# Performance work log

Measured on AMD Instinct MI355X. Metric: run time of the kernel, lower is better.

## Reference

```python
import jax, jax.numpy as jnp
import numpy as np

N, E, D, H = 100000, 20000, 64, 4
NNZ = 500000
NEG_SLOPE_ATT = 0.2   # PyG HypergraphConv attention leaky_relu slope
NEG_SLOPE_FFN = 0.01  # nn.LeakyReLU default
LN_EPS = 1e-5


def setup_inputs() -> dict:
    key = jax.random.key(0)
    ks = jax.random.split(key, 10)
    s = 0.05
    return {
        "x": jax.random.normal(ks[0], (N, D), jnp.float32),
        "adj_row": jax.random.randint(ks[1], (NNZ,), 0, N),
        "adj_col": jax.random.randint(ks[2], (NNZ,), 0, E),
        "adj_val": jax.random.uniform(ks[3], (NNZ,), jnp.float32) + 0.1,
        "num_edges": E,
        "lin_w": jax.random.normal(ks[4], (H * D, D), jnp.float32) * s,
        "att": jax.random.normal(ks[5], (1, H, 2 * D), jnp.float32) * s,
        "bias": jnp.zeros((D,), jnp.float32),
        "ln1_g": jnp.ones((D,), jnp.float32),
        "ln1_b": jnp.zeros((D,), jnp.float32),
        "ln2_g": jnp.ones((D,), jnp.float32),
        "ln2_b": jnp.zeros((D,), jnp.float32),
        "w1": jax.random.normal(ks[6], (D, D), jnp.float32) * s,
        "b1": jnp.zeros((D,), jnp.float32),
        "w2": jax.random.normal(ks[7], (D, D), jnp.float32) * s,
        "b2": jnp.zeros((D,), jnp.float32),
    }


def _layer_norm(x, g, b):
    mu = jnp.mean(x, axis=-1, keepdims=True)
    var = jnp.mean((x - mu) ** 2, axis=-1, keepdims=True)
    return (x - mu) * jax.lax.rsqrt(var + LN_EPS) * g + b


def _hypergraph_layer(x, adj_row, adj_col, adj_val, num_edges,
                      lin_w, att, bias, ln1_g, ln1_b, ln2_g, ln2_b,
                      w1, b1, w2, b2):
    n = x.shape[0]
    # --- get_hyperedge_representation: omega = diag(1/colsum) @ H^T @ x ---
    colsum = jax.ops.segment_sum(adj_val, adj_col, num_segments=num_edges)  # [E]
    omega = jax.ops.segment_sum(adj_val[:, None] * x[adj_row], adj_col,
                                num_segments=num_edges) / colsum[:, None]  # [E, D]
    # --- HypergraphConv (use_attention=True, concat=False) ---
    xh = (x @ lin_w.T).reshape(n, H, D)              # [N, H, D]
    eh = (omega @ lin_w.T).reshape(num_edges, H, D)  # [E, H, D]
    att_x, att_e = att[0, :, :D], att[0, :, D:]      # [H, D] each
    s_n = jnp.einsum('nhd,hd->nh', xh, att_x)        # [N, H]
    s_e = jnp.einsum('ehd,hd->eh', eh, att_e)        # [E, H]
    alpha = jax.nn.leaky_relu(s_n[adj_row] + s_e[adj_col], NEG_SLOPE_ATT)  # [NNZ, H]
    # softmax over incidences grouped by hyperedge (attention_mode='node')
    amax = jax.ops.segment_max(alpha, adj_col, num_segments=num_edges)
    ea = jnp.exp(alpha - amax[adj_col])
    alpha = ea / jax.ops.segment_sum(ea, adj_col, num_segments=num_edges)[adj_col]
    # degree normalizations D (node) and B (hyperedge)
    d_deg = jax.ops.segment_sum(adj_val[adj_col], adj_row, num_segments=n)
    d_inv = jnp.where(d_deg > 0, 1.0 / d_deg, 0.0)
    b_deg = jax.ops.segment_sum(jnp.ones_like(adj_val), adj_col, num_segments=num_edges)
    b_inv = jnp.where(b_deg > 0, 1.0 / b_deg, 0.0)
    # pass 1: nodes -> hyperedges  (norm_i = B at target edge)
    msg1 = b_inv[adj_col][:, None, None] * xh[adj_row] * alpha[:, :, None]
    edge_out = jax.ops.segment_sum(msg1, adj_col, num_segments=num_edges)  # [E,H,D]
    # pass 2: hyperedges -> nodes  (norm_i = D at target node)
    msg2 = d_inv[adj_row][:, None, None] * edge_out[adj_col] * alpha[:, :, None]
    node_out = jax.ops.segment_sum(msg2, adj_row, num_segments=n)  # [N,H,D]
    conv = jnp.mean(node_out, axis=1) + bias  # concat=False -> head mean
    # --- residual + norm + FFN (Linear, Linear, LeakyReLU) ---
    h = _layer_norm(x + conv, ln1_g, ln1_b)
    ffn = jax.nn.leaky_relu((h @ w1.T + b1) @ w2.T + b2, NEG_SLOPE_FFN)
    return _layer_norm(h + ffn, ln2_g, ln2_b)


def reference(x, adj_row, adj_col, adj_val, num_edges, lin_w, att, bias,
              ln1_g, ln1_b, ln2_g, ln2_b, w1, b1, w2, b2):
    return _hypergraph_layer(x, adj_row, adj_col, adj_val, num_edges,
                             lin_w, att, bias, ln1_g, ln1_b, ln2_g, ln2_b,
                             w1, b1, w2, b2)
```

## Files before the change

### kernel.cpp

```cpp
#include <hip/hip_runtime.h>

#define N_NODES 100000
#define N_EDGES 20000
#define DIM 64
#define HEADS 4
#define NNZ_ 500000
#define LNEPS 1e-5f

__device__ __forceinline__ float wsum64(float v){
#pragma unroll
  for (int off = 32; off; off >>= 1) v += __shfl_xor(v, off);
  return v;
}
__device__ __forceinline__ float wmax64(float v){
#pragma unroll
  for (int off = 32; off; off >>= 1) v = fmaxf(v, __shfl_xor(v, off));
  return v;
}
__device__ __forceinline__ float lrelu2(float a){ return a > 0.f ? a : 0.2f*a; }

__device__ __forceinline__ unsigned bfpack(float a, float b){
  unsigned ua = __float_as_uint(a), ub = __float_as_uint(b);
  ua += 0x7fffu + ((ua >> 16) & 1u);
  ub += 0x7fffu + ((ub >> 16) & 1u);
  return (ua >> 16) | (ub & 0xffff0000u);
}

__global__ __launch_bounds__(256) void k_hist(const int* __restrict__ row,
                                              const int* __restrict__ col,
                                              const float* __restrict__ val,
                                              int* __restrict__ ecnt, int* __restrict__ ncnt,
                                              float* __restrict__ colsum, float* __restrict__ ddeg){
  int i = blockIdx.x*256 + threadIdx.x;
  if (i >= NNZ_) return;
  int c = col[i], r = row[i];
  atomicAdd(&ecnt[c], 1);
  atomicAdd(&ncnt[r], 1);
  atomicAdd(&colsum[c], val[i]);
  atomicAdd(&ddeg[r], val[c]);
}

__global__ __launch_bounds__(1024) void k_scanA(const int* __restrict__ cnt,
                                                int* __restrict__ ptr,
                                                int* __restrict__ bsum, int n){
  __shared__ int wsums[16];
  int idx = blockIdx.x*1024 + threadIdx.x;
  int lane = threadIdx.x & 63, wid = threadIdx.x >> 6;
  int v = (idx < n) ? cnt[idx] : 0;
  int s = v;
#pragma unroll
  for (int off = 1; off < 64; off <<= 1){
    int t = __shfl_up(s, off);
    if (lane >= off) s += t;
  }
  if (lane == 63) wsums[wid] = s;
  __syncthreads();
  if (wid == 0 && lane < 16){
    int ws = wsums[lane];
    int t = ws;
#pragma unroll
    for (int off = 1; off < 16; off <<= 1){
      int u = __shfl_up(t, off);
      if (lane >= off) t += u;
    }
    wsums[lane] = t - ws;
  }
  __syncthreads();
  if (idx < n) ptr[idx] = wsums[wid] + s - v;
  if (threadIdx.x == 1023) bsum[blockIdx.x] = wsums[15] + s;
}

__global__ __launch_bounds__(256) void k_scanB(int* __restrict__ bsum, int nb,
                                               int* __restrict__ ptr, int n){
  __shared__ int sh[256];
  int t = threadIdx.x;
  int v = (t < nb) ? bsum[t] : 0;
  sh[t] = v;
  __syncthreads();
  for (int off = 1; off < 256; off <<= 1){
    int u = (t >= off) ? sh[t-off] : 0;
    __syncthreads();
    sh[t] += u;
    __syncthreads();
  }
  if (t < nb) bsum[t] = sh[t] - v;
  if (t == nb-1) ptr[n] = sh[t];
}

__global__ __launch_bounds__(1024) void k_scanC(int* __restrict__ ptr,
                                                const int* __restrict__ bsum, int n){
  int idx = blockIdx.x*1024 + threadIdx.x;
  if (idx < n) ptr[idx] += bsum[blockIdx.x];
}

__global__ __launch_bounds__(256) void k_scatter(const int* __restrict__ row,
                                                 const int* __restrict__ col,
                                                 const float* __restrict__ val,
                                                 const int* __restrict__ colptr,
                                                 const int* __restrict__ rowptr,
                                                 int* __restrict__ ecur, int* __restrict__ ncur,
                                                 int* __restrict__ rowC, float* __restrict__ valC,
                                                 int* __restrict__ rposC, int* __restrict__ colR){
  int i = blockIdx.x*256 + threadIdx.x;
  if (i >= NNZ_) return;
  int c = col[i], r = row[i];
  int p = atomicAdd(&ecur[c], 1);
  int q = atomicAdd(&ncur[r], 1);
  int cpos = colptr[c] + p;
  int rpos = rowptr[r] + q;
  rowC[cpos] = r;
  valC[cpos] = val[i];
  rposC[cpos] = rpos;
  colR[rpos] = c;
}

__global__ __launch_bounds__(256) void k_watt(const float* __restrict__ lin_w,
                                              const float* __restrict__ att,
                                              float* __restrict__ wattx,
                                              float* __restrict__ watte){
  int j = threadIdx.x;
  int h = j >> 6;
  float sx = 0.f, se = 0.f;
#pragma unroll
  for (int d = 0; d < DIM; ++d){
    float w = lin_w[(h*DIM + d)*DIM + (j & 63)];
    sx = fmaf(att[h*2*DIM + d],       w, sx);
    se = fmaf(att[h*2*DIM + DIM + d], w, se);
  }
  wattx[j] = sx;
  watte[j] = se;
}

__global__ __launch_bounds__(256) void k_wfold(const float* __restrict__ w1,
                                               const float* __restrict__ w2,
                                               const float* __restrict__ b1,
                                               const float* __restrict__ b2,
                                               float* __restrict__ Wf,
                                               float* __restrict__ bp){
  int tid = threadIdx.x;
#pragma unroll
  for (int m = 0; m < 16; ++m){
    int idx = m*256 + tid;
    int o = idx >> 6, k = idx & 63;
    float s = 0.f;
#pragma unroll
    for (int i = 0; i < 64; ++i)
      s = fmaf(w2[o*64 + i], w1[i*64 + k], s);
    Wf[idx] = s;
  }
  if (tid < 64){
    float s = b2[tid];
#pragma unroll
    for (int i = 0; i < 64; ++i)
      s = fmaf(w2[tid*64 + i], b1[i], s);
    bp[tid] = s;
  }
}

__global__ __launch_bounds__(256) void k_pre(const float* __restrict__ x,
                                             const float* __restrict__ wattx,
                                             const float* __restrict__ watte,
                                             float4* __restrict__ snpe){
  int lane = threadIdx.x & 63, wid = threadIdx.x >> 6;
  int n = blockIdx.x*4 + wid;
  if (n >= N_NODES) return;
  float xv = x[(size_t)n*DIM + lane];
  float s0 = wsum64(xv*wattx[lane]);
  float s1 = wsum64(xv*wattx[64+lane]);
  float s2 = wsum64(xv*wattx[128+lane]);
  float s3 = wsum64(xv*wattx[192+lane]);
  float p0 = wsum64(xv*watte[lane]);
  float p1 = wsum64(xv*watte[64+lane]);
  float p2 = wsum64(xv*watte[128+lane]);
  float p3 = wsum64(xv*watte[192+lane]);
  if (lane == 0){
    snpe[2*(size_t)n    ] = make_float4(s0,s1,s2,s3);
    snpe[2*(size_t)n + 1] = make_float4(p0,p1,p2,p3);
  }
}

__global__ __launch_bounds__(256) void k_softagg(const int* __restrict__ colptr,
                                                 const int* __restrict__ rowC,
                                                 const float* __restrict__ valC,
                                                 const int* __restrict__ rposC,
                                                 const float4* __restrict__ snpe,
                                                 const float* __restrict__ colsum,
                                                 const float* __restrict__ x,
                                                 float4* __restrict__ alphaC,
                                                 float4* __restrict__ alphaR,
                                                 float* __restrict__ agg){
  __shared__ float4 aSh[256];
  int lane = threadIdx.x & 63, wid = threadIdx.x >> 6;
  int e = blockIdx.x*4 + wid;
  if (e >= N_EDGES) return;
  int sb = __builtin_amdgcn_readfirstlane(colptr[e]);
  int cnt = __builtin_amdgcn_readfirstlane(colptr[e+1]) - sb;
  if (cnt == 0) return;
  float rcs = 1.0f / colsum[e];
  float acc0=0,acc1=0,acc2=0,acc3=0;

  if (cnt <= 64){
    bool act = lane < cnt;
    int r = 0, rp = 0; float v = 0.f;
    float4 snv = make_float4(0,0,0,0), p = make_float4(0,0,0,0);
    if (act){
      r = rowC[sb+lane];
      v = valC[sb+lane];
      rp = rposC[sb+lane];
      snv = snpe[2*(size_t)r];
      p   = snpe[2*(size_t)r + 1];
    }
    float se0 = wsum64(v*p.x)*rcs, se1 = wsum64(v*p.y)*rcs,
          se2 = wsum64(v*p.z)*rcs, se3 = wsum64(v*p.w)*rcs;
    float t0 = act ? lrelu2(snv.x+se0) : -1e30f;
    float t1 = act ? lrelu2(snv.y+se1) : -1e30f;
    float t2 = act ? lrelu2(snv.z+se2) : -1e30f;
    float t3 = act ? lrelu2(snv.w+se3) : -1e30f;
    float m0 = wmax64(t0), m1 = wmax64(t1), m2 = wmax64(t2), m3 = wmax64(t3);
    float e0 = act ? __expf(t0-m0) : 0.f;
    float e1 = act ? __expf(t1-m1) : 0.f;
    float e2 = act ? __expf(t2-m2) : 0.f;
    float e3 = act ? __expf(t3-m3) : 0.f;
    float q0 = wsum64(e0), q1 = wsum64(e1), q2 = wsum64(e2), q3 = wsum64(e3);
    float4 a = make_float4(e0/q0, e1/q1, e2/q2, e3/q3);
    if (act) alphaR[rp] = a;
    aSh[wid*64 + lane] = a;

    int k = 0;
    for (; k + 4 <= cnt; k += 4){
      int r0 = rowC[sb+k], r1 = rowC[sb+k+1], r2 = rowC[sb+k+2], r3 = rowC[sb+k+3];
      float4 a0 = aSh[wid*64+k], a1 = aSh[wid*64+k+1],
             a2 = aSh[wid*64+k+2], a3 = aSh[wid*64+k+3];
      float x0 = x[(size_t)r0*DIM + lane];
      float x1 = x[(size_t)r1*DIM + lane];
      float x2 = x[(size_t)r2*DIM + lane];
      float x3 = x[(size_t)r3*DIM + lane];
      acc0 = fmaf(a0.x, x0, acc0); acc1 = fmaf(a0.y, x0, acc1);
      acc2 = fmaf(a0.z, x0, acc2); acc3 = fmaf(a0.w, x0, acc3);
      acc0 = fmaf(a1.x, x1, acc0); acc1 = fmaf(a1.y, x1, acc1);
      acc2 = fmaf(a1.z, x1, acc2); acc3 = fmaf(a1.w, x1, acc3);
      acc0 = fmaf(a2.x, x2, acc0); acc1 = fmaf(a2.y, x2, acc1);
      acc2 = fmaf(a2.z, x2, acc2); acc3 = fmaf(a2.w, x2, acc3);
      acc0 = fmaf(a3.x, x3, acc0); acc1 = fmaf(a3.y, x3, acc1);
      acc2 = fmaf(a3.z, x3, acc2); acc3 = fmaf(a3.w, x3, acc3);
    }
    for (; k < cnt; ++k){
      int r0 = rowC[sb+k];
      float4 a0 = aSh[wid*64+k];
      float x0 = x[(size_t)r0*DIM + lane];
      acc0 = fmaf(a0.x, x0, acc0); acc1 = fmaf(a0.y, x0, acc1);
      acc2 = fmaf(a0.z, x0, acc2); acc3 = fmaf(a0.w, x0, acc3);
    }
  } else {
    int s = sb;
    float a0=0,a1=0,a2=0,a3=0;
    for (int base = 0; base < cnt; base += 64){
      int j = s + base + lane;
      if (base + lane < cnt){
        int r = rowC[j]; float v = valC[j];
        float4 p = snpe[2*(size_t)r + 1];
        a0 = fmaf(v,p.x,a0); a1 = fmaf(v,p.y,a1); a2 = fmaf(v,p.z,a2); a3 = fmaf(v,p.w,a3);
      }
    }
    float se0 = wsum64(a0)*rcs, se1 = wsum64(a1)*rcs, se2 = wsum64(a2)*rcs, se3 = wsum64(a3)*rcs;
    float m0=-1e30f,m1=-1e30f,m2=-1e30f,m3=-1e30f;
    for (int base = 0; base < cnt; base += 64){
      int j = s + base + lane;
      if (base + lane < cnt){
        float4 snv = snpe[2*(size_t)rowC[j]];
        m0 = fmaxf(m0, lrelu2(snv.x+se0)); m1 = fmaxf(m1, lrelu2(snv.y+se1));
        m2 = fmaxf(m2, lrelu2(snv.z+se2)); m3 = fmaxf(m3, lrelu2(snv.w+se3));
      }
    }
    m0 = wmax64(m0); m1 = wmax64(m1); m2 = wmax64(m2); m3 = wmax64(m3);
    float q0=0,q1=0,q2=0,q3=0;
    for (int base = 0; base < cnt; base += 64){
      int j = s + base + lane;
      if (base + lane < cnt){
        float4 snv = snpe[2*(size_t)rowC[j]];
        float e0 = __expf(lrelu2(snv.x+se0)-m0), e1 = __expf(lrelu2(snv.y+se1)-m1);
        float e2 = __expf(lrelu2(snv.z+se2)-m2), e3 = __expf(lrelu2(snv.w+se3)-m3);
        q0+=e0; q1+=e1; q2+=e2; q3+=e3;
        alphaC[j] = make_float4(e0,e1,e2,e3);
      }
    }
    q0 = wsum64(q0); q1 = wsum64(q1); q2 = wsum64(q2); q3 = wsum64(q3);
    float r0 = 1.f/q0, r1 = 1.f/q1, r2 = 1.f/q2, r3 = 1.f/q3;
    for (int base = 0; base < cnt; base += 64){
      int j = s + base + lane;
      if (base + lane < cnt){
        float4 av = alphaC[j];
        av = make_float4(av.x*r0, av.y*r1, av.z*r2, av.w*r3);
        alphaC[j] = av;
        alphaR[rposC[j]] = av;
      }
    }
    for (int k = 0; k < cnt; ++k){
      int rj = rowC[sb+k];
      float4 al = alphaC[sb+k];
      float xv = x[(size_t)rj*DIM + lane];
      acc0 = fmaf(al.x, xv, acc0); acc1 = fmaf(al.y, xv, acc1);
      acc2 = fmaf(al.z, xv, acc2); acc3 = fmaf(al.w, xv, acc3);
    }
  }

  float binv = 1.0f/(float)cnt;
  size_t b = (size_t)e*256;
  agg[b       + lane] = acc0*binv;
  agg[b +  64 + lane] = acc1*binv;
  agg[b + 128 + lane] = acc2*binv;
  agg[b + 192 + lane] = acc3*binv;
}

__global__ __launch_bounds__(256) void k_eoT(const float* __restrict__ agg,
                                             const float* __restrict__ lin_w,
                                             unsigned short* __restrict__ eoTb){
  __shared__ float L[16*260];
  int lane = threadIdx.x & 63, h = threadIdx.x >> 6;
  float w[64];
  const float4* wr = (const float4*)(lin_w + ((size_t)h*64 + lane)*64);
#pragma unroll
  for (int k = 0; k < 16; ++k){
    float4 t = wr[k];
    w[4*k] = t.x; w[4*k+1] = t.y; w[4*k+2] = t.z; w[4*k+3] = t.w;
  }
  int e0 = blockIdx.x*16;
  for (int el = 0; el < 16; ++el){
    float av = agg[(size_t)(e0+el)*256 + h*64 + lane];
    float o = 0.f;
#pragma unroll
    for (int k = 0; k < 64; ++k) o = fmaf(__shfl(av, k), w[k], o);
    L[el*260 + lane*4 + h] = o;
  }
  __syncthreads();
  int tid = threadIdx.x;
#pragma unroll
  for (int p = 0; p < 4; ++p){
    int el = p*4 + (tid >> 6);
    int l = tid & 63;
    const float* Lr = &L[el*260 + l*4];
    uint2 v;
    v.x = bfpack(Lr[0], Lr[1]);
    v.y = bfpack(Lr[2], Lr[3]);
    *(uint2*)(eoTb + (size_t)(e0+el)*256 + l*4) = v;
  }
}

#define ACC4(J, V, A) { \
  float u0 = __uint_as_float((V).x << 16); \
  float u1 = __uint_as_float((V).x & 0xffff0000u); \
  float u2 = __uint_as_float((V).y << 16); \
  float u3 = __uint_as_float((V).y & 0xffff0000u); \
  acc[J][0] = fmaf(u0, (A).x, acc[J][0]); \
  acc[J][1] = fmaf(u1, (A).y, acc[J][1]); \
  acc[J][2] = fmaf(u2, (A).z, acc[J][2]); \
  acc[J][3] = fmaf(u3, (A).w, acc[J][3]); }

#define SEG(J, KB, KE) do { \
    int k = (KB); \
    for (; k + 4 <= (KE); k += 4){ \
      int c0 = colR[k], c1 = colR[k+1], c2 = colR[k+2], c3 = colR[k+3]; \
      float4 a0 = alphaR[k], a1 = alphaR[k+1], a2 = alphaR[k+2], a3 = alphaR[k+3]; \
      uint2 v0 = *(const uint2*)(eoTb + (size_t)c0*256 + lane*4); \
      uint2 v1 = *(const uint2*)(eoTb + (size_t)c1*256 + lane*4); \
      uint2 v2 = *(const uint2*)(eoTb + (size_t)c2*256 + lane*4); \
      uint2 v3 = *(const uint2*)(eoTb + (size_t)c3*256 + lane*4); \
      ACC4(J, v0, a0); ACC4(J, v1, a1); ACC4(J, v2, a2); ACC4(J, v3, a3); \
    } \
    for (; k < (KE); ++k){ \
      int c0 = colR[k]; float4 a0 = alphaR[k]; \
      uint2 v0 = *(const uint2*)(eoTb + (size_t)c0*256 + lane*4); \
      ACC4(J, v0, a0); \
    } \
  } while(0)

__global__ __launch_bounds__(256) void k_final2(const float* __restrict__ x,
                                                const int* __restrict__ rowptr,
                                                const int* __restrict__ colR,
                                                const float4* __restrict__ alphaR,
                                                const unsigned short* __restrict__ eoTb,
                                                const float* __restrict__ ddeg,
                                                const float* __restrict__ bias,
                                                const float* __restrict__ g1,
                                                const float* __restrict__ b1g,
                                                const float* __restrict__ g2,
                                                const float* __restrict__ b2g,
                                                const float* __restrict__ Wf,
                                                const float* __restrict__ bp,
                                                float* __restrict__ out){
  int lane = threadIdx.x & 63, wid = threadIdx.x >> 6;
  int nbase = blockIdx.x*16 + wid*4;
  int q0 = __builtin_amdgcn_readfirstlane(rowptr[nbase]);
  int q1 = __builtin_amdgcn_readfirstlane(rowptr[nbase+1]);
  int q2 = __builtin_amdgcn_readfirstlane(rowptr[nbase+2]);
  int q3 = __builtin_amdgcn_readfirstlane(rowptr[nbase+3]);
  int q4 = __builtin_amdgcn_readfirstlane(rowptr[nbase+4]);

  float xv[4];
#pragma unroll
  for (int j = 0; j < 4; ++j) xv[j] = x[(size_t)(nbase+j)*DIM + lane];
  float dd0 = ddeg[nbase], dd1 = ddeg[nbase+1], dd2 = ddeg[nbase+2], dd3 = ddeg[nbase+3];
  float w[64];
  const float4* wr = (const float4*)(Wf + (size_t)lane*64);
#pragma unroll
  for (int k = 0; k < 16; ++k){
    float4 t = wr[k];
    w[4*k] = t.x; w[4*k+1] = t.y; w[4*k+2] = t.z; w[4*k+3] = t.w;
  }
  float biasv = bias[lane], bpv = bp[lane];
  float g1v = g1[lane], b1gv = b1g[lane], g2v = g2[lane], b2gv = b2g[lane];

  float acc[4][4];
#pragma unroll
  for (int j = 0; j < 4; ++j)
#pragma unroll
    for (int h = 0; h < 4; ++h) acc[j][h] = 0.f;

  SEG(0, q0, q1);
  SEG(1, q1, q2);
  SEG(2, q2, q3);
  SEG(3, q3, q4);

  float ddv[4] = {dd0, dd1, dd2, dd3};
  float hs[4];
#pragma unroll
  for (int j = 0; j < 4; ++j){
    float dd = ddv[j];
    float dinv = dd > 0.f ? 0.25f/dd : 0.f;
    float conv = (acc[j][0]+acc[j][1]+acc[j][2]+acc[j][3])*dinv;
    float t = xv[j] + conv + biasv;
    float mu = wsum64(t) * (1.f/64.f);
    float dv = t - mu;
    float var = wsum64(dv*dv) * (1.f/64.f);
    hs[j] = dv * rsqrtf(var + LNEPS) * g1v + b1gv;
  }

  float a0 = bpv, a1 = bpv, a2 = bpv, a3 = bpv;
#pragma unroll
  for (int k = 0; k < 64; ++k){
    a0 = fmaf(__shfl(hs[0], k), w[k], a0);
    a1 = fmaf(__shfl(hs[1], k), w[k], a1);
    a2 = fmaf(__shfl(hs[2], k), w[k], a2);
    a3 = fmaf(__shfl(hs[3], k), w[k], a3);
  }

  float fa[4] = {a0, a1, a2, a3};
#pragma unroll
  for (int j = 0; j < 4; ++j){
    int n = nbase + j;
    float ffn = fa[j] > 0.f ? fa[j] : 0.01f*fa[j];
    float t2 = hs[j] + ffn;
    float mu2 = wsum64(t2) * (1.f/64.f);
    float dv2 = t2 - mu2;
    float var2 = wsum64(dv2*dv2) * (1.f/64.f);
    out[(size_t)n*DIM + lane] = dv2 * rsqrtf(var2 + LNEPS) * g2v + b2gv;
  }
}

extern "C" void kernel_launch(void* const* d_in, const int* in_sizes, int n_in,
                              void* d_out, int out_size, void* d_ws, size_t ws_size,
                              hipStream_t stream){
  const float* x     = (const float*)d_in[0];
  const int*   row   = (const int*)d_in[1];
  const int*   col   = (const int*)d_in[2];
  const float* val   = (const float*)d_in[3];
  const float* lin_w = (const float*)d_in[5];
  const float* att   = (const float*)d_in[6];
  const float* bias  = (const float*)d_in[7];
  const float* g1    = (const float*)d_in[8];
  const float* b1g   = (const float*)d_in[9];
  const float* g2    = (const float*)d_in[10];
  const float* b2g   = (const float*)d_in[11];
  const float* w1    = (const float*)d_in[12];
  const float* b1    = (const float*)d_in[13];
  const float* w2    = (const float*)d_in[14];
  const float* b2    = (const float*)d_in[15];
  float* out = (float*)d_out;
  float* ws  = (float*)d_ws;

  constexpr size_t E = N_EDGES, Nn = N_NODES;
  constexpr size_t o_ecnt   = 0;
  constexpr size_t o_ncnt   = o_ecnt + E;
  constexpr size_t o_ecur   = o_ncnt + Nn;
  constexpr size_t o_ncur   = o_ecur + E;
  constexpr size_t o_colsum = o_ncur + Nn;
  constexpr size_t o_ddeg   = o_colsum + E;
  constexpr size_t ZEND     = o_ddeg + Nn;
  constexpr size_t o_colptr = ZEND;
  constexpr size_t o_rowptr = o_colptr + E + 4;
  constexpr size_t o_bsumE  = o_rowptr + Nn + 4;
  constexpr size_t o_bsumN  = o_bsumE + 256;
  constexpr size_t o_rowC   = o_bsumN + 256;
  constexpr size_t o_valC   = o_rowC + NNZ_;
  constexpr size_t o_rposC  = o_valC + NNZ_;
  constexpr size_t o_colR   = o_rposC + NNZ_;
  constexpr size_t o_wattx  = o_colR + NNZ_;
  constexpr size_t o_watte  = o_wattx + 256;
  constexpr size_t o_Wf     = o_watte + 256;
  constexpr size_t o_bp     = o_Wf + 4096;
  constexpr size_t o_snpe   = o_bp + 64;
  constexpr size_t o_alphaC = o_snpe + 8*Nn;
  constexpr size_t o_alphaR = o_alphaC + 4*(size_t)NNZ_;
  constexpr size_t o_agg    = o_alphaR + 4*(size_t)NNZ_;
  constexpr size_t o_eo     = o_agg + 256*E;

  int*    ecnt   = (int*)(ws + o_ecnt);
  int*    ncnt   = (int*)(ws + o_ncnt);
  int*    ecur   = (int*)(ws + o_ecur);
  int*    ncur   = (int*)(ws + o_ncur);
  float*  colsum = ws + o_colsum;
  float*  ddeg   = ws + o_ddeg;
  int*    colptr = (int*)(ws + o_colptr);
  int*    rowptr = (int*)(ws + o_rowptr);
  int*    bsumE  = (int*)(ws + o_bsumE);
  int*    bsumN  = (int*)(ws + o_bsumN);
  int*    rowC   = (int*)(ws + o_rowC);
  float*  valC   = ws + o_valC;
  int*    rposC  = (int*)(ws + o_rposC);
  int*    colR   = (int*)(ws + o_colR);
  float*  wattx  = ws + o_wattx;
  float*  watte  = ws + o_watte;
  float*  Wf     = ws + o_Wf;
  float*  bp     = ws + o_bp;
  float4* snpe   = (float4*)(ws + o_snpe);
  float4* alphaC = (float4*)(ws + o_alphaC);
  float4* alphaR = (float4*)(ws + o_alphaR);
  float*  agg    = ws + o_agg;
  unsigned short* eoTb = (unsigned short*)(ws + o_eo);

  hipMemsetAsync(ws, 0, ZEND*sizeof(float), stream);

  k_hist<<<(NNZ_+255)/256, 256, 0, stream>>>(row, col, val, ecnt, ncnt, colsum, ddeg);

  int nbE = (int)((E + 1023)/1024);
  int nbN = (int)((Nn + 1023)/1024);
  k_scanA<<<nbE, 1024, 0, stream>>>(ecnt, colptr, bsumE, (int)E);
  k_scanB<<<1, 256, 0, stream>>>(bsumE, nbE, colptr, (int)E);
  k_scanC<<<nbE, 1024, 0, stream>>>(colptr, bsumE, (int)E);
  k_scanA<<<nbN, 1024, 0, stream>>>(ncnt, rowptr, bsumN, (int)Nn);
  k_scanB<<<1, 256, 0, stream>>>(bsumN, nbN, rowptr, (int)Nn);
  k_scanC<<<nbN, 1024, 0, stream>>>(rowptr, bsumN, (int)Nn);

  k_scatter<<<(NNZ_+255)/256, 256, 0, stream>>>(row, col, val, colptr, rowptr,
                                                ecur, ncur, rowC, valC, rposC, colR);

  k_watt<<<1, 256, 0, stream>>>(lin_w, att, wattx, watte);
  k_wfold<<<1, 256, 0, stream>>>(w1, w2, b1, b2, Wf, bp);
  k_pre<<<(int)((Nn+3)/4), 256, 0, stream>>>(x, wattx, watte, snpe);
  k_softagg<<<(int)((E+3)/4), 256, 0, stream>>>(colptr, rowC, valC, rposC, snpe, colsum,
                                                x, alphaC, alphaR, agg);
  k_eoT<<<(int)(E/16), 256, 0, stream>>>(agg, lin_w, eoTb);
  k_final2<<<(int)(Nn/16), 256, 0, stream>>>(x, rowptr, colR, alphaR, eoTb, ddeg,
                                             bias, g1, b1g, g2, b2g, Wf, bp, out);
}
```

Before: 452.6 us.

## Merge edge/node scan launches, unroll eoT over 4 edges, one node per wave in final

The separate edge and node prefix-scan kernels are merged into three combined launches, which cuts launch count and serialization. k_eoT now processes four edges per inner iteration so one weight register value feeds four FMAs. k_final2 switches from four nodes per wave to one node per wave with four times as many blocks. This exposes more parallelism and balances load across irregular row lengths, at the cost of reloading the 64-float weight row per node instead of amortizing it over four.

```diff
diff --git a/kernel.cpp b/kernel.cpp
--- a/kernel.cpp
+++ b/kernel.cpp
@@ -40,11 +40,10 @@
   atomicAdd(&ddeg[r], val[c]);
 }
 
-__global__ __launch_bounds__(1024) void k_scanA(const int* __restrict__ cnt,
-                                                int* __restrict__ ptr,
-                                                int* __restrict__ bsum, int n){
+__device__ __forceinline__ void scanA_body(const int* cnt, int* ptr, int* bsum,
+                                           int n, int blk){
   __shared__ int wsums[16];
-  int idx = blockIdx.x*1024 + threadIdx.x;
+  int idx = blk*1024 + threadIdx.x;
   int lane = threadIdx.x & 63, wid = threadIdx.x >> 6;
   int v = (idx < n) ? cnt[idx] : 0;
   int s = v;
@@ -67,11 +66,21 @@
   }
   __syncthreads();
   if (idx < n) ptr[idx] = wsums[wid] + s - v;
-  if (threadIdx.x == 1023) bsum[blockIdx.x] = wsums[15] + s;
-}
-
-__global__ __launch_bounds__(256) void k_scanB(int* __restrict__ bsum, int nb,
-                                               int* __restrict__ ptr, int n){
+  if (threadIdx.x == 1023) bsum[blk] = wsums[15] + s;
+}
+
+__global__ __launch_bounds__(1024) void k_scanA2(const int* __restrict__ ecnt,
+                                                 int* __restrict__ colptr,
+                                                 int* __restrict__ bsumE, int nbE,
+                                                 const int* __restrict__ ncnt,
+                                                 int* __restrict__ rowptr,
+                                                 int* __restrict__ bsumN){
+  int b = blockIdx.x;
+  if (b < nbE) scanA_body(ecnt, colptr, bsumE, N_EDGES, b);
+  else         scanA_body(ncnt, rowptr, bsumN, N_NODES, b - nbE);
+}
+
+__device__ __forceinline__ void scanB_body(int* bsum, int nb, int* ptr, int n){
   __shared__ int sh[256];
   int t = threadIdx.x;
   int v = (t < nb) ? bsum[t] : 0;
@@ -87,10 +96,26 @@
   if (t == nb-1) ptr[n] = sh[t];
 }
 
-__global__ __launch_bounds__(1024) void k_scanC(int* __restrict__ ptr,
-                                                const int* __restrict__ bsum, int n){
-  int idx = blockIdx.x*1024 + threadIdx.x;
-  if (idx < n) ptr[idx] += bsum[blockIdx.x];
+__global__ __launch_bounds__(256) void k_scanB2(int* __restrict__ bsumE, int nbE,
+                                                int* __restrict__ colptr,
+                                                int* __restrict__ bsumN, int nbN,
+                                                int* __restrict__ rowptr){
+  if (blockIdx.x == 0) scanB_body(bsumE, nbE, colptr, N_EDGES);
+  else                 scanB_body(bsumN, nbN, rowptr, N_NODES);
+}
+
+__global__ __launch_bounds__(1024) void k_scanC2(int* __restrict__ colptr,
+                                                 const int* __restrict__ bsumE, int nbE,
+                                                 int* __restrict__ rowptr,
+                                                 const int* __restrict__ bsumN){
+  int b = blockIdx.x;
+  if (b < nbE){
+    int idx = b*1024 + threadIdx.x;
+    if (idx < N_EDGES) colptr[idx] += bsumE[b];
+  } else {
+    int idx = (b - nbE)*1024 + threadIdx.x;
+    if (idx < N_NODES) rowptr[idx] += bsumN[b - nbE];
+  }
 }
 
 __global__ __launch_bounds__(256) void k_scatter(const int* __restrict__ row,
@@ -325,12 +350,25 @@
     w[4*k] = t.x; w[4*k+1] = t.y; w[4*k+2] = t.z; w[4*k+3] = t.w;
   }
   int e0 = blockIdx.x*16;
-  for (int el = 0; el < 16; ++el){
-    float av = agg[(size_t)(e0+el)*256 + h*64 + lane];
-    float o = 0.f;
-#pragma unroll
-    for (int k = 0; k < 64; ++k) o = fmaf(__shfl(av, k), w[k], o);
-    L[el*260 + lane*4 + h] = o;
+#pragma unroll
+  for (int el = 0; el < 16; el += 4){
+    float av0 = agg[(size_t)(e0+el  )*256 + h*64 + lane];
+    float av1 = agg[(size_t)(e0+el+1)*256 + h*64 + lane];
+    float av2 = agg[(size_t)(e0+el+2)*256 + h*64 + lane];
+    float av3 = agg[(size_t)(e0+el+3)*256 + h*64 + lane];
+    float o0=0.f, o1=0.f, o2=0.f, o3=0.f;
+#pragma unroll
+    for (int k = 0; k < 64; ++k){
+      float wk = w[k];
+      o0 = fmaf(__shfl(av0, k), wk, o0);
+      o1 = fmaf(__shfl(av1, k), wk, o1);
+      o2 = fmaf(__shfl(av2, k), wk, o2);
+      o3 = fmaf(__shfl(av3, k), wk, o3);
+    }
+    L[(el  )*260 + lane*4 + h] = o0;
+    L[(el+1)*260 + lane*4 + h] = o1;
+    L[(el+2)*260 + lane*4 + h] = o2;
+    L[(el+3)*260 + lane*4 + h] = o3;
   }
   __syncthreads();
   int tid = threadIdx.x;
@@ -346,33 +384,15 @@
   }
 }
 
-#define ACC4(J, V, A) { \
+#define ACC1(V, A) { \
   float u0 = __uint_as_float((V).x << 16); \
   float u1 = __uint_as_float((V).x & 0xffff0000u); \
   float u2 = __uint_as_float((V).y << 16); \
   float u3 = __uint_as_float((V).y & 0xffff0000u); \
-  acc[J][0] = fmaf(u0, (A).x, acc[J][0]); \
-  acc[J][1] = fmaf(u1, (A).y, acc[J][1]); \
-  acc[J][2] = fmaf(u2, (A).z, acc[J][2]); \
-  acc[J][3] = fmaf(u3, (A).w, acc[J][3]); }
-
-#define SEG(J, KB, KE) do { \
-    int k = (KB); \
-    for (; k + 4 <= (KE); k += 4){ \
-      int c0 = colR[k], c1 = colR[k+1], c2 = colR[k+2], c3 = colR[k+3]; \
-      float4 a0 = alphaR[k], a1 = alphaR[k+1], a2 = alphaR[k+2], a3 = alphaR[k+3]; \
-      uint2 v0 = *(const uint2*)(eoTb + (size_t)c0*256 + lane*4); \
-      uint2 v1 = *(const uint2*)(eoTb + (size_t)c1*256 + lane*4); \
-      uint2 v2 = *(const uint2*)(eoTb + (size_t)c2*256 + lane*4); \
-      uint2 v3 = *(const uint2*)(eoTb + (size_t)c3*256 + lane*4); \
-      ACC4(J, v0, a0); ACC4(J, v1, a1); ACC4(J, v2, a2); ACC4(J, v3, a3); \
-    } \
-    for (; k < (KE); ++k){ \
-      int c0 = colR[k]; float4 a0 = alphaR[k]; \
-      uint2 v0 = *(const uint2*)(eoTb + (size_t)c0*256 + lane*4); \
-      ACC4(J, v0, a0); \
-    } \
-  } while(0)
+  acc0 = fmaf(u0, (A).x, acc0); \
+  acc1 = fmaf(u1, (A).y, acc1); \
+  acc2 = fmaf(u2, (A).z, acc2); \
+  acc3 = fmaf(u3, (A).w, acc3); }
 
 __global__ __launch_bounds__(256) void k_final2(const float* __restrict__ x,
                                                 const int* __restrict__ rowptr,
@@ -389,72 +409,59 @@
                                                 const float* __restrict__ bp,
                                                 float* __restrict__ out){
   int lane = threadIdx.x & 63, wid = threadIdx.x >> 6;
-  int nbase = blockIdx.x*16 + wid*4;
-  int q0 = __builtin_amdgcn_readfirstlane(rowptr[nbase]);
-  int q1 = __builtin_amdgcn_readfirstlane(rowptr[nbase+1]);
-  int q2 = __builtin_amdgcn_readfirstlane(rowptr[nbase+2]);
-  int q3 = __builtin_amdgcn_readfirstlane(rowptr[nbase+3]);
-  int q4 = __builtin_amdgcn_readfirstlane(rowptr[nbase+4]);
-
-  float xv[4];
-#pragma unroll
-  for (int j = 0; j < 4; ++j) xv[j] = x[(size_t)(nbase+j)*DIM + lane];
-  float dd0 = ddeg[nbase], dd1 = ddeg[nbase+1], dd2 = ddeg[nbase+2], dd3 = ddeg[nbase+3];
+  int n = blockIdx.x*4 + wid;
+  int q0 = __builtin_amdgcn_readfirstlane(rowptr[n]);
+  int q1 = __builtin_amdgcn_readfirstlane(rowptr[n+1]);
+
+  float xv = x[(size_t)n*DIM + lane];
+  float dd = ddeg[n];
+
+  float acc0=0.f, acc1=0.f, acc2=0.f, acc3=0.f;
+  int k = q0;
+  for (; k + 4 <= q1; k += 4){
+    int c0 = colR[k], c1 = colR[k+1], c2 = colR[k+2], c3 = colR[k+3];
+    float4 a0 = alphaR[k], a1 = alphaR[k+1], a2 = alphaR[k+2], a3 = alphaR[k+3];
+    uint2 v0 = *(const uint2*)(eoTb + (size_t)c0*256 + lane*4);
+    uint2 v1 = *(const uint2*)(eoTb + (size_t)c1*256 + lane*4);
+    uint2 v2 = *(const uint2*)(eoTb + (size_t)c2*256 + lane*4);
+    uint2 v3 = *(const uint2*)(eoTb + (size_t)c3*256 + lane*4);
+    ACC1(v0, a0); ACC1(v1, a1); ACC1(v2, a2); ACC1(v3, a3);
+  }
+  for (; k < q1; ++k){
+    int c0 = colR[k]; float4 a0 = alphaR[k];
+    uint2 v0 = *(const uint2*)(eoTb + (size_t)c0*256 + lane*4);
+    ACC1(v0, a0);
+  }
+
   float w[64];
   const float4* wr = (const float4*)(Wf + (size_t)lane*64);
 #pragma unroll
-  for (int k = 0; k < 16; ++k){
-    float4 t = wr[k];
-    w[4*k] = t.x; w[4*k+1] = t.y; w[4*k+2] = t.z; w[4*k+3] = t.w;
+  for (int kk = 0; kk < 16; ++kk){
+    float4 t = wr[kk];
+    w[4*kk] = t.x; w[4*kk+1] = t.y; w[4*kk+2] = t.z; w[4*kk+3] = t.w;
   }
   float biasv = bias[lane], bpv = bp[lane];
   float g1v = g1[lane], b1gv = b1g[lane], g2v = g2[lane], b2gv = b2g[lane];
 
-  float acc[4][4];
-#pragma unroll
-  for (int j = 0; j < 4; ++j)
-#pragma unroll
-    for (int h = 0; h < 4; ++h) acc[j][h] = 0.f;
-
-  SEG(0, q0, q1);
-  SEG(1, q1, q2);
-  SEG(2, q2, q3);
-  SEG(3, q3, q4);
-
-  float ddv[4] = {dd0, dd1, dd2, dd3};
-  float hs[4];
-#pragma unroll
-  for (int j = 0; j < 4; ++j){
-    float dd = ddv[j];
-    float dinv = dd > 0.f ? 0.25f/dd : 0.f;
-    float conv = (acc[j][0]+acc[j][1]+acc[j][2]+acc[j][3])*dinv;
-    float t = xv[j] + conv + biasv;
-    float mu = wsum64(t) * (1.f/64.f);
-    float dv = t - mu;
-    float var = wsum64(dv*dv) * (1.f/64.f);
-    hs[j] = dv * rsqrtf(var + LNEPS) * g1v + b1gv;
-  }
-
-  float a0 = bpv, a1 = bpv, a2 = bpv, a3 = bpv;
-#pragma unroll
-  for (int k = 0; k < 64; ++k){
-    a0 = fmaf(__shfl(hs[0], k), w[k], a0);
-    a1 = fmaf(__shfl(hs[1], k), w[k], a1);
-    a2 = fmaf(__shfl(hs[2], k), w[k], a2);
-    a3 = fmaf(__shfl(hs[3], k), w[k], a3);
-  }
-
-  float fa[4] = {a0, a1, a2, a3};
-#pragma unroll
-  for (int j = 0; j < 4; ++j){
-    int n = nbase + j;
-    float ffn = fa[j] > 0.f ? fa[j] : 0.01f*fa[j];
-    float t2 = hs[j] + ffn;
-    float mu2 = wsum64(t2) * (1.f/64.f);
-    float dv2 = t2 - mu2;
-    float var2 = wsum64(dv2*dv2) * (1.f/64.f);
-    out[(size_t)n*DIM + lane] = dv2 * rsqrtf(var2 + LNEPS) * g2v + b2gv;
-  }
+  float dinv = dd > 0.f ? 0.25f/dd : 0.f;
+  float conv = (acc0+acc1+acc2+acc3)*dinv;
+  float t = xv + conv + biasv;
+  float mu = wsum64(t) * (1.f/64.f);
+  float dv = t - mu;
+  float var = wsum64(dv*dv) * (1.f/64.f);
+  float hv = dv * rsqrtf(var + LNEPS) * g1v + b1gv;
+
+  float a = bpv;
+#pragma unroll
+  for (int kk = 0; kk < 64; ++kk)
+    a = fmaf(__shfl(hv, kk), w[kk], a);
+
+  float ffn = a > 0.f ? a : 0.01f*a;
+  float t2 = hv + ffn;
+  float mu2 = wsum64(t2) * (1.f/64.f);
+  float dv2 = t2 - mu2;
+  float var2 = wsum64(dv2*dv2) * (1.f/64.f);
+  out[(size_t)n*DIM + lane] = dv2 * rsqrtf(var2 + LNEPS) * g2v + b2gv;
 }
 
 extern "C" void kernel_launch(void* const* d_in, const int* in_sizes, int n_in,
@@ -534,12 +541,9 @@
 
   int nbE = (int)((E + 1023)/1024);
   int nbN = (int)((Nn + 1023)/1024);
-  k_scanA<<<nbE, 1024, 0, stream>>>(ecnt, colptr, bsumE, (int)E);
-  k_scanB<<<1, 256, 0, stream>>>(bsumE, nbE, colptr, (int)E);
-  k_scanC<<<nbE, 1024, 0, stream>>>(colptr, bsumE, (int)E);
-  k_scanA<<<nbN, 1024, 0, stream>>>(ncnt, rowptr, bsumN, (int)Nn);
-  k_scanB<<<1, 256, 0, stream>>>(bsumN, nbN, rowptr, (int)Nn);
-  k_scanC<<<nbN, 1024, 0, stream>>>(rowptr, bsumN, (int)Nn);
+  k_scanA2<<<nbE + nbN, 1024, 0, stream>>>(ecnt, colptr, bsumE, nbE, ncnt, rowptr, bsumN);
+  k_scanB2<<<2, 256, 0, stream>>>(bsumE, nbE, colptr, bsumN, nbN, rowptr);
+  k_scanC2<<<nbE + nbN, 1024, 0, stream>>>(colptr, bsumE, nbE, rowptr, bsumN);
 
   k_scatter<<<(NNZ_+255)/256, 256, 0, stream>>>(row, col, val, colptr, rowptr,
                                                 ecur, ncur, rowC, valC, rposC, colR);
@@ -550,6 +554,6 @@
   k_softagg<<<(int)((E+3)/4), 256, 0, stream>>>(colptr, rowC, valC, rposC, snpe, colsum,
                                                 x, alphaC, alphaR, agg);
   k_eoT<<<(int)(E/16), 256, 0, stream>>>(agg, lin_w, eoTb);
-  k_final2<<<(int)(Nn/16), 256, 0, stream>>>(x, rowptr, colR, alphaR, eoTb, ddeg,
-                                             bias, g1, b1g, g2, b2g, Wf, bp, out);
-}
+  k_final2<<<(int)(Nn/4), 256, 0, stream>>>(x, rowptr, colR, alphaR, eoTb, ddeg,
+                                            bias, g1, b1g, g2, b2g, Wf, bp, out);
+}
```

Result: slower. 548.8 us (+21.3%).

## Merge scan kernels, shrink block sizes, unroll eoT over four edges

Applied to the files above, without the earlier changes.

Fuses the separate edge and node prefix-scan launches into three combined kernels, cutting the launch count from six to three. Halves the block size of k_pre, k_softagg and k_final2 so more, smaller blocks are scheduled. Reworks k_eoT to process four edges per inner loop, reusing each weight register across them. Moves the Wf register load in k_final2 after the gather loop to shorten register live ranges. The extra accumulators in k_eoT raise register pressure, and smaller blocks add scheduling overhead.

```diff
diff --git a/kernel.cpp b/kernel.cpp
--- a/kernel.cpp
+++ b/kernel.cpp
@@ -40,11 +40,10 @@
   atomicAdd(&ddeg[r], val[c]);
 }
 
-__global__ __launch_bounds__(1024) void k_scanA(const int* __restrict__ cnt,
-                                                int* __restrict__ ptr,
-                                                int* __restrict__ bsum, int n){
+__device__ __forceinline__ void scanA_body(const int* cnt, int* ptr, int* bsum,
+                                           int n, int blk){
   __shared__ int wsums[16];
-  int idx = blockIdx.x*1024 + threadIdx.x;
+  int idx = blk*1024 + threadIdx.x;
   int lane = threadIdx.x & 63, wid = threadIdx.x >> 6;
   int v = (idx < n) ? cnt[idx] : 0;
   int s = v;
@@ -67,11 +66,21 @@
   }
   __syncthreads();
   if (idx < n) ptr[idx] = wsums[wid] + s - v;
-  if (threadIdx.x == 1023) bsum[blockIdx.x] = wsums[15] + s;
-}
-
-__global__ __launch_bounds__(256) void k_scanB(int* __restrict__ bsum, int nb,
-                                               int* __restrict__ ptr, int n){
+  if (threadIdx.x == 1023) bsum[blk] = wsums[15] + s;
+}
+
+__global__ __launch_bounds__(1024) void k_scanA2(const int* __restrict__ ecnt,
+                                                 int* __restrict__ colptr,
+                                                 int* __restrict__ bsumE, int nbE,
+                                                 const int* __restrict__ ncnt,
+                                                 int* __restrict__ rowptr,
+                                                 int* __restrict__ bsumN){
+  int b = blockIdx.x;
+  if (b < nbE) scanA_body(ecnt, colptr, bsumE, N_EDGES, b);
+  else         scanA_body(ncnt, rowptr, bsumN, N_NODES, b - nbE);
+}
+
+__device__ __forceinline__ void scanB_body(int* bsum, int nb, int* ptr, int n){
   __shared__ int sh[256];
   int t = threadIdx.x;
   int v = (t < nb) ? bsum[t] : 0;
@@ -87,10 +96,26 @@
   if (t == nb-1) ptr[n] = sh[t];
 }
 
-__global__ __launch_bounds__(1024) void k_scanC(int* __restrict__ ptr,
-                                                const int* __restrict__ bsum, int n){
-  int idx = blockIdx.x*1024 + threadIdx.x;
-  if (idx < n) ptr[idx] += bsum[blockIdx.x];
+__global__ __launch_bounds__(256) void k_scanB2(int* __restrict__ bsumE, int nbE,
+                                                int* __restrict__ colptr,
+                                                int* __restrict__ bsumN, int nbN,
+                                                int* __restrict__ rowptr){
+  if (blockIdx.x == 0) scanB_body(bsumE, nbE, colptr, N_EDGES);
+  else                 scanB_body(bsumN, nbN, rowptr, N_NODES);
+}
+
+__global__ __launch_bounds__(1024) void k_scanC2(int* __restrict__ colptr,
+                                                 const int* __restrict__ bsumE, int nbE,
+                                                 int* __restrict__ rowptr,
+                                                 const int* __restrict__ bsumN){
+  int b = blockIdx.x;
+  if (b < nbE){
+    int idx = b*1024 + threadIdx.x;
+    if (idx < N_EDGES) colptr[idx] += bsumE[b];
+  } else {
+    int idx = (b - nbE)*1024 + threadIdx.x;
+    if (idx < N_NODES) rowptr[idx] += bsumN[b - nbE];
+  }
 }
 
 __global__ __launch_bounds__(256) void k_scatter(const int* __restrict__ row,
@@ -157,12 +182,12 @@
   }
 }
 
-__global__ __launch_bounds__(256) void k_pre(const float* __restrict__ x,
+__global__ __launch_bounds__(128) void k_pre(const float* __restrict__ x,
                                              const float* __restrict__ wattx,
                                              const float* __restrict__ watte,
                                              float4* __restrict__ snpe){
   int lane = threadIdx.x & 63, wid = threadIdx.x >> 6;
-  int n = blockIdx.x*4 + wid;
+  int n = blockIdx.x*2 + wid;
   if (n >= N_NODES) return;
   float xv = x[(size_t)n*DIM + lane];
   float s0 = wsum64(xv*wattx[lane]);
@@ -179,7 +204,7 @@
   }
 }
 
-__global__ __launch_bounds__(256) void k_softagg(const int* __restrict__ colptr,
+__global__ __launch_bounds__(128) void k_softagg(const int* __restrict__ colptr,
                                                  const int* __restrict__ rowC,
                                                  const float* __restrict__ valC,
                                                  const int* __restrict__ rposC,
@@ -189,9 +214,9 @@
                                                  float4* __restrict__ alphaC,
                                                  float4* __restrict__ alphaR,
                                                  float* __restrict__ agg){
-  __shared__ float4 aSh[256];
+  __shared__ float4 aSh[128];
   int lane = threadIdx.x & 63, wid = threadIdx.x >> 6;
-  int e = blockIdx.x*4 + wid;
+  int e = blockIdx.x*2 + wid;
   if (e >= N_EDGES) return;
   int sb = __builtin_amdgcn_readfirstlane(colptr[e]);
   int cnt = __builtin_amdgcn_readfirstlane(colptr[e+1]) - sb;
@@ -325,12 +350,25 @@
     w[4*k] = t.x; w[4*k+1] = t.y; w[4*k+2] = t.z; w[4*k+3] = t.w;
   }
   int e0 = blockIdx.x*16;
-  for (int el = 0; el < 16; ++el){
-    float av = agg[(size_t)(e0+el)*256 + h*64 + lane];
-    float o = 0.f;
-#pragma unroll
-    for (int k = 0; k < 64; ++k) o = fmaf(__shfl(av, k), w[k], o);
-    L[el*260 + lane*4 + h] = o;
+#pragma unroll
+  for (int el = 0; el < 16; el += 4){
+    float av0 = agg[(size_t)(e0+el  )*256 + h*64 + lane];
+    float av1 = agg[(size_t)(e0+el+1)*256 + h*64 + lane];
+    float av2 = agg[(size_t)(e0+el+2)*256 + h*64 + lane];
+    float av3 = agg[(size_t)(e0+el+3)*256 + h*64 + lane];
+    float o0=0.f, o1=0.f, o2=0.f, o3=0.f;
+#pragma unroll
+    for (int k = 0; k < 64; ++k){
+      float wk = w[k];
+      o0 = fmaf(__shfl(av0, k), wk, o0);
+      o1 = fmaf(__shfl(av1, k), wk, o1);
+      o2 = fmaf(__shfl(av2, k), wk, o2);
+      o3 = fmaf(__shfl(av3, k), wk, o3);
+    }
+    L[(el  )*260 + lane*4 + h] = o0;
+    L[(el+1)*260 + lane*4 + h] = o1;
+    L[(el+2)*260 + lane*4 + h] = o2;
+    L[(el+3)*260 + lane*4 + h] = o3;
   }
   __syncthreads();
   int tid = threadIdx.x;
@@ -374,7 +412,7 @@
     } \
   } while(0)
 
-__global__ __launch_bounds__(256) void k_final2(const float* __restrict__ x,
+__global__ __launch_bounds__(128) void k_final2(const float* __restrict__ x,
                                                 const int* __restrict__ rowptr,
                                                 const int* __restrict__ colR,
                                                 const float4* __restrict__ alphaR,
@@ -389,7 +427,7 @@
                                                 const float* __restrict__ bp,
                                                 float* __restrict__ out){
   int lane = threadIdx.x & 63, wid = threadIdx.x >> 6;
-  int nbase = blockIdx.x*16 + wid*4;
+  int nbase = blockIdx.x*8 + wid*4;
   int q0 = __builtin_amdgcn_readfirstlane(rowptr[nbase]);
   int q1 = __builtin_amdgcn_readfirstlane(rowptr[nbase+1]);
   int q2 = __builtin_amdgcn_readfirstlane(rowptr[nbase+2]);
@@ -400,15 +438,6 @@
 #pragma unroll
   for (int j = 0; j < 4; ++j) xv[j] = x[(size_t)(nbase+j)*DIM + lane];
   float dd0 = ddeg[nbase], dd1 = ddeg[nbase+1], dd2 = ddeg[nbase+2], dd3 = ddeg[nbase+3];
-  float w[64];
-  const float4* wr = (const float4*)(Wf + (size_t)lane*64);
-#pragma unroll
-  for (int k = 0; k < 16; ++k){
-    float4 t = wr[k];
-    w[4*k] = t.x; w[4*k+1] = t.y; w[4*k+2] = t.z; w[4*k+3] = t.w;
-  }
-  float biasv = bias[lane], bpv = bp[lane];
-  float g1v = g1[lane], b1gv = b1g[lane], g2v = g2[lane], b2gv = b2g[lane];
 
   float acc[4][4];
 #pragma unroll
@@ -420,6 +449,16 @@
   SEG(1, q1, q2);
   SEG(2, q2, q3);
   SEG(3, q3, q4);
+
+  float w[64];
+  const float4* wr = (const float4*)(Wf + (size_t)lane*64);
+#pragma unroll
+  for (int k = 0; k < 16; ++k){
+    float4 t = wr[k];
+    w[4*k] = t.x; w[4*k+1] = t.y; w[4*k+2] = t.z; w[4*k+3] = t.w;
+  }
+  float biasv = bias[lane], bpv = bp[lane];
+  float g1v = g1[lane], b1gv = b1g[lane], g2v = g2[lane], b2gv = b2g[lane];
 
   float ddv[4] = {dd0, dd1, dd2, dd3};
   float hs[4];
@@ -534,22 +573,19 @@
 
   int nbE = (int)((E + 1023)/1024);
   int nbN = (int)((Nn + 1023)/1024);
-  k_scanA<<<nbE, 1024, 0, stream>>>(ecnt, colptr, bsumE, (int)E);
-  k_scanB<<<1, 256, 0, stream>>>(bsumE, nbE, colptr, (int)E);
-  k_scanC<<<nbE, 1024, 0, stream>>>(colptr, bsumE, (int)E);
-  k_scanA<<<nbN, 1024, 0, stream>>>(ncnt, rowptr, bsumN, (int)Nn);
-  k_scanB<<<1, 256, 0, stream>>>(bsumN, nbN, rowptr, (int)Nn);
-  k_scanC<<<nbN, 1024, 0, stream>>>(rowptr, bsumN, (int)Nn);
+  k_scanA2<<<nbE + nbN, 1024, 0, stream>>>(ecnt, colptr, bsumE, nbE, ncnt, rowptr, bsumN);
+  k_scanB2<<<2, 256, 0, stream>>>(bsumE, nbE, colptr, bsumN, nbN, rowptr);
+  k_scanC2<<<nbE + nbN, 1024, 0, stream>>>(colptr, bsumE, nbE, rowptr, bsumN);
 
   k_scatter<<<(NNZ_+255)/256, 256, 0, stream>>>(row, col, val, colptr, rowptr,
                                                 ecur, ncur, rowC, valC, rposC, colR);
 
   k_watt<<<1, 256, 0, stream>>>(lin_w, att, wattx, watte);
   k_wfold<<<1, 256, 0, stream>>>(w1, w2, b1, b2, Wf, bp);
-  k_pre<<<(int)((Nn+3)/4), 256, 0, stream>>>(x, wattx, watte, snpe);
-  k_softagg<<<(int)((E+3)/4), 256, 0, stream>>>(colptr, rowC, valC, rposC, snpe, colsum,
+  k_pre<<<(int)((Nn+1)/2), 128, 0, stream>>>(x, wattx, watte, snpe);
+  k_softagg<<<(int)((E+1)/2), 128, 0, stream>>>(colptr, rowC, valC, rposC, snpe, colsum,
                                                 x, alphaC, alphaR, agg);
   k_eoT<<<(int)(E/16), 256, 0, stream>>>(agg, lin_w, eoTb);
-  k_final2<<<(int)(Nn/16), 256, 0, stream>>>(x, rowptr, colR, alphaR, eoTb, ddeg,
-                                             bias, g1, b1g, g2, b2g, Wf, bp, out);
-}
+  k_final2<<<(int)(Nn/8), 128, 0, stream>>>(x, rowptr, colR, alphaR, eoTb, ddeg,
+                                            bias, g1, b1g, g2, b2g, Wf, bp, out);
+}
```

Measured after the change: 456.5 us. No clear change (+0.9%).
